# Optimization experiments

Measured on AMD Instinct MI355X. Metric: run time of the kernel, lower is better.

Reference implementation:

```python
import jax, jax.numpy as jnp
import numpy as np

B, SA, SB, H, D = 1, 2048, 512, 24, 128
DIM = H * D
EPS = 1e-6


def rms_norm(x, w):
    # fp32 variance as in the torch module (inputs already fp32 here)
    var = jnp.mean(jnp.square(x.astype(jnp.float32)), axis=-1, keepdims=True)
    y = (x * jax.lax.rsqrt(var + EPS)).astype(x.dtype)
    return y * w


def apply_rope(x, freqs):
    # x: [B,H,S,D]; freqs: [1,1,S,D/2,2,2]
    x_ = x.astype(jnp.float32).reshape(*x.shape[:-1], -1, 1, 2)  # [B,H,S,D/2,1,2]
    out = freqs[..., 0] * x_[..., 0] + freqs[..., 1] * x_[..., 1]  # [B,H,S,D/2,2]
    return out.reshape(x.shape).astype(x.dtype)


def qkv_split(x, W, b):
    # x: [B,S,DIM] -> q,k,v each [B,H,S,D]; chunk(3,dim=1) on 3H axis == major-3 split
    qkv = (x @ W + b).reshape(x.shape[0], x.shape[1], 3, H, D)
    qkv = jnp.transpose(qkv, (2, 0, 3, 1, 4))  # [3,B,H,S,D]
    return qkv[0], qkv[1], qkv[2]


def setup_inputs():
    key = jax.random.key(0)
    ks = jax.random.split(key, 8)
    s = 0.02
    return {
        "hidden_states_a": jax.random.normal(ks[0], (B, SA, DIM), jnp.float32),
        "hidden_states_b": jax.random.normal(ks[1], (B, SB, DIM), jnp.float32),
        "image_rotary_emb": jax.random.normal(ks[2], (1, 1, SA + SB, D // 2, 2, 2), jnp.float32),
        "Wqkv_a": jax.random.normal(ks[3], (DIM, 3 * DIM), jnp.float32) * s,
        "bqkv_a": jnp.zeros((3 * DIM,), jnp.float32),
        "Wqkv_b": jax.random.normal(ks[4], (DIM, 3 * DIM), jnp.float32) * s,
        "bqkv_b": jnp.zeros((3 * DIM,), jnp.float32),
        "wq_a": jnp.ones((D,), jnp.float32),
        "wk_a": jnp.ones((D,), jnp.float32),
        "wq_b": jnp.ones((D,), jnp.float32),
        "wk_b": jnp.ones((D,), jnp.float32),
        "Wout_a": jax.random.normal(ks[5], (DIM, DIM), jnp.float32) * s,
        "bout_a": jnp.zeros((DIM,), jnp.float32),
        "Wout_b": jax.random.normal(ks[6], (DIM, DIM), jnp.float32) * s,
        "bout_b": jnp.zeros((DIM,), jnp.float32),
    }


def reference(hidden_states_a, hidden_states_b, image_rotary_emb,
              Wqkv_a, bqkv_a, Wqkv_b, bqkv_b,
              wq_a, wk_a, wq_b, wk_b,
              Wout_a, bout_a, Wout_b, bout_b):
    q_a, k_a, v_a = qkv_split(hidden_states_a, Wqkv_a, bqkv_a)
    q_a, k_a = rms_norm(q_a, wq_a), rms_norm(k_a, wk_a)
    q_b, k_b, v_b = qkv_split(hidden_states_b, Wqkv_b, bqkv_b)
    q_b, k_b = rms_norm(q_b, wq_b), rms_norm(k_b, wk_b)

    q = jnp.concatenate([q_b, q_a], axis=2)
    k = jnp.concatenate([k_b, k_a], axis=2)
    v = jnp.concatenate([v_b, v_a], axis=2)
    q, k = apply_rope(q, image_rotary_emb), apply_rope(k, image_rotary_emb)

    scale = 1.0 / jnp.sqrt(jnp.asarray(D, q.dtype))
    scores = jnp.einsum("bhqd,bhkd->bhqk", q, k) * scale
    attn = jax.nn.softmax(scores, axis=-1)
    out = jnp.einsum("bhqk,bhkd->bhqd", attn, v)
    out = jnp.transpose(out, (0, 2, 1, 3)).reshape(B, SA + SB, DIM)

    out_b, out_a = out[:, :SB], out[:, SB:]
    hidden_states_a = out_a @ Wout_a + bout_a
    hidden_states_b = out_b @ Wout_b + bout_b
    return hidden_states_a, hidden_states_b
```

## Files before the change

### kernel.cpp

```cpp
#include <hip/hip_runtime.h>
#include <hip/hip_bf16.h>


typedef __attribute__((ext_vector_type(8))) short s16x8;
typedef __attribute__((ext_vector_type(8))) unsigned short u16x8;
typedef __attribute__((ext_vector_type(4))) float f32x4;
typedef __attribute__((ext_vector_type(16))) float f32x16;

#define DEV static __device__ __forceinline__

#define S_TOT 2560
#define DIMC 3072
#define NQKV 9216

DEV unsigned short f2bf(float f) {
  union { float f; unsigned u; } v; v.f = f;
  return (unsigned short)((v.u + 0x7fffu + ((v.u >> 16) & 1u)) >> 16);
}
DEV float bf2f(unsigned short h) {
  union { unsigned u; float f; } v; v.u = ((unsigned)h) << 16;
  return v.f;
}
DEV void gload16(const void* g, void* l) {
  __builtin_amdgcn_global_load_lds((__attribute__((address_space(1))) void*)g,
                                   (__attribute__((address_space(3))) void*)l,
                                   16, 0, 0);
}
DEV float exp2_fast(float x) {
#if __has_builtin(__builtin_amdgcn_exp2f)
  return __builtin_amdgcn_exp2f(x);
#else
  return __expf(x * 0.69314718056f);
#endif
}
template <int CTRL>
DEV float dppf(float x) {
  return __int_as_float(__builtin_amdgcn_update_dpp(0, __float_as_int(x), CTRL, 0xf, 0xf, true));
}
DEV float rowmax16(float x) {
  x = fmaxf(x, dppf<0xB1>(x));
  x = fmaxf(x, dppf<0x4E>(x));
  x = fmaxf(x, dppf<0x141>(x));
  x = fmaxf(x, dppf<0x140>(x));
  return x;
}
DEV float rowsum16(float x) {
  x += dppf<0xB1>(x);
  x += dppf<0x4E>(x);
  x += dppf<0x141>(x);
  x += dppf<0x140>(x);
  return x;
}

DEV void tile_map(int t, int mgrid, int* m, int* n) {
  int sg = t >> 4, loc = t & 15;
  int mgs = mgrid >> 2;
  int mg = sg % mgs, ng = sg / mgs;
  *m = mg * 4 + (loc & 3);
  *n = ng * 4 + (loc >> 2);
}


__global__ __launch_bounds__(256) void cvt_bf16_k(const float* __restrict__ in,
                                                  unsigned short* __restrict__ out,
                                                  int n8) {
  int i = blockIdx.x * 256 + threadIdx.x;
  if (i >= n8) return;
  const float4* p = (const float4*)(in + (size_t)i * 8);
  float4 a = p[0], b = p[1];
  u16x8 u;
  u[0] = f2bf(a.x); u[1] = f2bf(a.y); u[2] = f2bf(a.z); u[3] = f2bf(a.w);
  u[4] = f2bf(b.x); u[5] = f2bf(b.y); u[6] = f2bf(b.z); u[7] = f2bf(b.w);
  *(u16x8*)(out + (size_t)i * 8) = u;
}

__global__ __launch_bounds__(256) void transpose_cvt(const float* __restrict__ W,
                                                     unsigned short* __restrict__ WT,
                                                     int K, int N) {
  __shared__ float tile[64][65];
  const int t = threadIdx.x;
  const int n0 = blockIdx.x * 64, k0 = blockIdx.y * 64;
#pragma unroll
  for (int rep = 0; rep < 4; ++rep) {
    int idx = rep * 256 + t;
    int r = idx >> 4, c4 = (idx & 15) * 4;
    float4 v = *(const float4*)&W[(size_t)(k0 + r) * N + n0 + c4];
    tile[r][c4] = v.x; tile[r][c4 + 1] = v.y; tile[r][c4 + 2] = v.z; tile[r][c4 + 3] = v.w;
  }
  __syncthreads();
#pragma unroll
  for (int rep = 0; rep < 2; ++rep) {
    int idx = rep * 256 + t;
    int j = idx >> 3, i0 = (idx & 7) * 8;
    u16x8 u;
#pragma unroll
    for (int i = 0; i < 8; i++) u[i] = f2bf(tile[i0 + i][j]);
    *(u16x8*)&WT[(size_t)(n0 + j) * K + k0 + i0] = u;
  }
}


struct StageSmem {
  unsigned short A[128 * 64];
  unsigned short B[128 * 64];
};

DEV void stage_tile(const char* A, const char* B, StageSmem* s, int kt, int tid) {
  const int row_s = tid >> 3;
  const int kbp = (tid & 7) * 16;
#pragma unroll
  for (int st = 0; st < 4; ++st) {
    int row = st * 32 + row_s;
    int kb = kbp ^ ((row & 7) << 4);
    gload16(A + (size_t)row * (DIMC * 2) + kt * 128 + kb, (char*)s->A + st * 4096 + tid * 16);
    gload16(B + (size_t)row * (DIMC * 2) + kt * 128 + kb, (char*)s->B + st * 4096 + tid * 16);
  }
}

DEV void gemm_core(const unsigned short* __restrict__ Ap,
                   const unsigned short* __restrict__ Bp,
                   StageSmem (&sm)[2], int tid, f32x4 (&acc)[4][4]) {
  const int wave = tid >> 6, lane = tid & 63;
  const int wr = wave >> 1, wc = wave & 1;
  const int lh = lane >> 4, ll = lane & 15;

  stage_tile((const char*)Ap, (const char*)Bp, &sm[0], 0, tid);
  __syncthreads();

  for (int kt = 0; kt < 48; ++kt) {
    if (kt + 1 < 48)
      stage_tile((const char*)Ap, (const char*)Bp, &sm[(kt + 1) & 1], kt + 1, tid);
    const StageSmem* s = &sm[kt & 1];
#pragma unroll
    for (int ks = 0; ks < 2; ++ks) {
      s16x8 a[4], b[4];
#pragma unroll
      for (int f = 0; f < 4; ++f) {
        int ar = wr * 64 + f * 16 + ll;
        a[f] = *(const s16x8*)((const char*)s->A + ar * 128 +
                               ((ks * 64 + lh * 16) ^ ((ar & 7) << 4)));
        int br = wc * 64 + f * 16 + ll;
        b[f] = *(const s16x8*)((const char*)s->B + br * 128 +
                               ((ks * 64 + lh * 16) ^ ((br & 7) << 4)));
      }
#pragma unroll
      for (int i = 0; i < 4; i++)
#pragma unroll
        for (int j = 0; j < 4; j++)
          acc[i][j] = __builtin_amdgcn_mfma_f32_16x16x32_bf16(a[i], b[j], acc[i][j], 0, 0, 0);
    }
    __syncthreads();
  }
}


union QkvSmem {
  StageSmem st[2];
  unsigned short ctile[128 * 136];
};

__global__ __launch_bounds__(256, 2) void qkv_gemm(
    const unsigned short* __restrict__ X0, const unsigned short* __restrict__ X1,
    const unsigned short* __restrict__ W0, const unsigned short* __restrict__ W1,
    const float* __restrict__ b0, const float* __restrict__ b1,
    const float* __restrict__ wqa, const float* __restrict__ wka,
    const float* __restrict__ wqb, const float* __restrict__ wkb,
    const float* __restrict__ freqs,
    unsigned short* __restrict__ Qb, unsigned short* __restrict__ Kb,
    unsigned short* __restrict__ Vt, int nt0) {
  __shared__ QkvSmem sm;
  const int tid = threadIdx.x;

  const int chunk = gridDim.x >> 3;
  const int nid = ((int)blockIdx.x & 7) * chunk + ((int)blockIdx.x >> 3);
  const int strm = (nid >= nt0) ? 1 : 0;
  const int t = strm ? nid - nt0 : nid;
  int mt, nt;
  tile_map(t, strm ? 4 : 16, &mt, &nt);
  const int m0 = mt * 128, n0 = nt * 128;
  const unsigned short* Xp = (strm ? X1 : X0) + (size_t)m0 * DIMC;
  const unsigned short* Wp = (strm ? W1 : W0) + (size_t)n0 * DIMC;
  const float* biasp = (strm ? b1 : b0);
  const int s_off = strm ? 0 : 512;

  f32x4 acc[4][4] = {};
  gemm_core(Xp, Wp, sm.st, tid, acc);

  {
    const int wave = tid >> 6, lane = tid & 63;
    const int wr = wave >> 1, wc = wave & 1, lh = lane >> 4, ll = lane & 15;
#pragma unroll
    for (int fn = 0; fn < 4; ++fn) {
      int c = wc * 64 + fn * 16 + ll;
      float bv = biasp[n0 + c];
#pragma unroll
      for (int fm = 0; fm < 4; ++fm)
#pragma unroll
        for (int j = 0; j < 4; j++) {
          int r = wr * 64 + fm * 16 + lh * 4 + j;
          sm.ctile[r * 136 + c] = f2bf(acc[fm][fn][j] + bv);
        }
    }
  }
  __syncthreads();

  const int qkv_idx = nt / 24;
  const int head = nt % 24;

  if (qkv_idx == 2) {
    const int sg0 = s_off + m0;
#pragma unroll
    for (int half = 0; half < 2; ++half) {
      int d = half * 64 + (tid >> 2);
      int t0 = (tid & 3) * 32;
      size_t obase = (size_t)(head * 128 + d) * S_TOT + sg0 + t0;
#pragma unroll
      for (int v = 0; v < 4; ++v) {
        u16x8 u;
#pragma unroll
        for (int i = 0; i < 8; i++) u[i] = sm.ctile[(t0 + v * 8 + i) * 136 + d];
        *(u16x8*)&Vt[obase + v * 8] = u;
      }
    }
  } else {
    const float* wn = (qkv_idx == 0) ? (strm ? wqb : wqa) : (strm ? wkb : wka);
    unsigned short* Ob = (qkv_idx == 0) ? Qb : Kb;
    const int row = tid >> 1, half = tid & 1;
    const int sg = s_off + m0 + row;
    float x[64];
    float ss = 0.f;
#pragma unroll
    for (int i = 0; i < 64; i++) {
      float v = bf2f(sm.ctile[row * 136 + half * 64 + i]);
      x[i] = v; ss += v * v;
    }
    ss += __shfl_xor(ss, 1);
    const float rn = rsqrtf(ss * (1.f / 128.f) + 1e-6f);
    const float* fr = freqs + (size_t)sg * 256 + half * 128;
    unsigned short o[64];
#pragma unroll
    for (int p = 0; p < 32; ++p) {
      float w0 = wn[half * 64 + 2 * p], w1 = wn[half * 64 + 2 * p + 1];
      float y0 = x[2 * p] * rn * w0, y1 = x[2 * p + 1] * rn * w1;
      float f00 = fr[p * 4], f01 = fr[p * 4 + 1], f10 = fr[p * 4 + 2], f11 = fr[p * 4 + 3];
      o[2 * p] = f2bf(f00 * y0 + f01 * y1);
      o[2 * p + 1] = f2bf(f10 * y0 + f11 * y1);
    }
    size_t ob = ((size_t)head * S_TOT + sg) * 128 + half * 64;
#pragma unroll
    for (int v = 0; v < 8; ++v) {
      u16x8 u;
#pragma unroll
      for (int i = 0; i < 8; i++) u[i] = o[v * 8 + i];
      *(u16x8*)&Ob[ob + v * 8] = u;
    }
  }
}


__global__ __launch_bounds__(256, 2) void out_gemm(
    const unsigned short* __restrict__ A0, const unsigned short* __restrict__ A1,
    const unsigned short* __restrict__ W0, const unsigned short* __restrict__ W1,
    const float* __restrict__ b0, const float* __restrict__ b1,
    float* __restrict__ C0, float* __restrict__ C1, int nt0) {
  __shared__ StageSmem sm[2];
  const int tid = threadIdx.x;
  const int chunk = gridDim.x >> 3;
  const int nid = ((int)blockIdx.x & 7) * chunk + ((int)blockIdx.x >> 3);
  const int strm = (nid >= nt0) ? 1 : 0;
  const int t = strm ? nid - nt0 : nid;
  int mt, nt;
  tile_map(t, strm ? 4 : 16, &mt, &nt);
  const int m0 = mt * 128, n0 = nt * 128;
  const unsigned short* Ap = (strm ? A1 : A0) + (size_t)m0 * DIMC;
  const unsigned short* Wp = (strm ? W1 : W0) + (size_t)n0 * DIMC;
  const float* bias = strm ? b1 : b0;
  float* C = strm ? C1 : C0;

  f32x4 acc[4][4] = {};
  gemm_core(Ap, Wp, sm, tid, acc);
  const int wave = tid >> 6, lane = tid & 63;
  const int wr = wave >> 1, wc = wave & 1, lh = lane >> 4, ll = lane & 15;
#pragma unroll
  for (int fn = 0; fn < 4; ++fn) {
    int c = n0 + wc * 64 + fn * 16 + ll;
    float bv = bias[c];
#pragma unroll
    for (int fm = 0; fm < 4; ++fm)
#pragma unroll
      for (int j = 0; j < 4; j++) {
        int r = m0 + wr * 64 + fm * 16 + lh * 4 + j;
        C[(size_t)r * DIMC + c] = acc[fm][fn][j] + bv;
      }
  }
}


__global__ __launch_bounds__(256, 2) void attn_k(
    const unsigned short* __restrict__ Qb, const unsigned short* __restrict__ Kb,
    const unsigned short* __restrict__ Vt, unsigned short* __restrict__ AO) {
  __shared__ alignas(128) unsigned short Ks[2][64 * 128];
  __shared__ alignas(128) unsigned short Vs[128 * 64];
  __shared__ alignas(128) unsigned short Ps[4][32 * 72];
  __shared__ float tabA[4][32];
  __shared__ float tabL[4][32];

  const int tid = threadIdx.x, w = tid >> 6, lane = tid & 63;
  const int lh = lane >> 4, ll16 = lane & 15;
  const int ll31 = lane & 31, hi = lane >> 5;
  const int wgid = blockIdx.x;
  const int nid = (wgid & 7) * 60 + (wgid >> 3);
  const int h = nid / 20, qt = nid % 20;
  const float C = 0.12751744f;

  s16x8 qf[2][4];
#pragma unroll
  for (int rb = 0; rb < 2; rb++) {
    size_t qbase = ((size_t)h * S_TOT + qt * 128 + w * 32 + rb * 16 + ll16) * 128;
#pragma unroll
    for (int ks = 0; ks < 4; ks++) qf[rb][ks] = *(const s16x8*)&Qb[qbase + ks * 32 + lh * 8];
  }

  float m2[2][4], l_r[2][4];
  f32x16 o[4] = {};
#pragma unroll
  for (int rb = 0; rb < 2; rb++)
#pragma unroll
    for (int j = 0; j < 4; j++) { m2[rb][j] = -1e30f; l_r[rb][j] = 0.f; }

  const unsigned short* Kh = Kb + (size_t)h * S_TOT * 128;
  const unsigned short* Vh = Vt + (size_t)h * 128 * S_TOT;
  unsigned short* Pw = &Ps[w][0];

  {
#pragma unroll
    for (int st = 0; st < 4; ++st) {
      int row = st * 16 + (tid >> 4);
      int col = ((tid & 15) * 16) ^ ((row & 7) << 4);
      gload16((const char*)(Kh + (size_t)row * 128) + col,
              (char*)&Ks[0][0] + st * 4096 + tid * 16);
    }
  }

  int cur = 0;
  for (int kt = 0; kt < 40; ++kt) {
    __syncthreads();
    {
      const int k0 = kt * 64;
#pragma unroll
      for (int st = 0; st < 4; ++st) {
        int row = st * 32 + (tid >> 3);
        int col = ((tid & 7) * 16) ^ ((row & 7) << 4);
        gload16((const char*)(Vh + (size_t)row * S_TOT + k0) + col,
                (char*)Vs + st * 4096 + tid * 16);
      }
    }
    if (kt + 1 < 40) {
      const unsigned short* Kn = Kh + (size_t)(kt + 1) * 64 * 128;
#pragma unroll
      for (int st = 0; st < 4; ++st) {
        int row = st * 16 + (tid >> 4);
        int col = ((tid & 15) * 16) ^ ((row & 7) << 4);
        gload16((const char*)(Kn + (size_t)row * 128) + col,
                (char*)&Ks[cur ^ 1][0] + st * 4096 + tid * 16);
      }
    }

    const char* Kc = (const char*)&Ks[cur][0];
    f32x4 sc[2][4] = {};
#pragma unroll
    for (int kb = 0; kb < 4; kb++) {
      int krow = kb * 16 + ll16;
      const char* kr = Kc + krow * 256;
      int swz = (krow & 7) << 4;
#pragma unroll
      for (int ks = 0; ks < 4; ks++) {
        s16x8 bf = *(const s16x8*)(kr + ((ks * 64 + lh * 16) ^ swz));
        sc[0][kb] = __builtin_amdgcn_mfma_f32_16x16x32_bf16(qf[0][ks], bf, sc[0][kb], 0, 0, 0);
        sc[1][kb] = __builtin_amdgcn_mfma_f32_16x16x32_bf16(qf[1][ks], bf, sc[1][kb], 0, 0, 0);
      }
    }

    float pmax[2][4];
#pragma unroll
    for (int rb = 0; rb < 2; rb++)
#pragma unroll
      for (int j = 0; j < 4; j++) {
        float v = fmaxf(fmaxf(sc[rb][0][j], sc[rb][1][j]), fmaxf(sc[rb][2][j], sc[rb][3][j]));
        pmax[rb][j] = rowmax16(v) * C;
      }
    bool need = false;
#pragma unroll
    for (int rb = 0; rb < 2; rb++)
#pragma unroll
      for (int j = 0; j < 4; j++) need |= (pmax[rb][j] > m2[rb][j] + 8.0f);
    if (__any(need)) {
#pragma unroll
      for (int rb = 0; rb < 2; rb++)
#pragma unroll
        for (int j = 0; j < 4; j++) {
          float mn = fmaxf(m2[rb][j], pmax[rb][j]);
          float al = exp2_fast(m2[rb][j] - mn);
          m2[rb][j] = mn;
          l_r[rb][j] *= al;
          if (ll16 == 0) tabA[w][rb * 16 + lh * 4 + j] = al;
        }
#pragma unroll
      for (int reg = 0; reg < 16; reg++) {
        int cr = (reg & 3) + 8 * (reg >> 2) + 4 * hi;
        float alv = tabA[w][cr];
        o[0][reg] *= alv; o[1][reg] *= alv; o[2][reg] *= alv; o[3][reg] *= alv;
      }
    }
#pragma unroll
    for (int rb = 0; rb < 2; rb++) {
      float ps0 = 0.f, ps1 = 0.f, ps2 = 0.f, ps3 = 0.f;
#pragma unroll
      for (int kb = 0; kb < 4; kb++) {
        float p0 = exp2_fast(sc[rb][kb][0] * C - m2[rb][0]);
        float p1 = exp2_fast(sc[rb][kb][1] * C - m2[rb][1]);
        float p2 = exp2_fast(sc[rb][kb][2] * C - m2[rb][2]);
        float p3 = exp2_fast(sc[rb][kb][3] * C - m2[rb][3]);
        ps0 += p0; ps1 += p1; ps2 += p2; ps3 += p3;
        int rbase = (rb * 16 + lh * 4);
        Pw[(rbase + 0) * 72 + kb * 16 + ll16] = f2bf(p0);
        Pw[(rbase + 1) * 72 + kb * 16 + ll16] = f2bf(p1);
        Pw[(rbase + 2) * 72 + kb * 16 + ll16] = f2bf(p2);
        Pw[(rbase + 3) * 72 + kb * 16 + ll16] = f2bf(p3);
      }
      l_r[rb][0] += rowsum16(ps0);
      l_r[rb][1] += rowsum16(ps1);
      l_r[rb][2] += rowsum16(ps2);
      l_r[rb][3] += rowsum16(ps3);
    }

    __syncthreads();

#pragma unroll
    for (int kstep = 0; kstep < 4; kstep++) {
      s16x8 pa = *(const s16x8*)((const char*)Pw + ll31 * 144 + kstep * 32 + hi * 16);
#pragma unroll
      for (int dblk = 0; dblk < 4; dblk++) {
        int vrow = dblk * 32 + ll31;
        s16x8 vb = *(const s16x8*)((const char*)Vs + vrow * 128 +
                                   ((kstep * 32 + hi * 16) ^ ((vrow & 7) << 4)));
        o[dblk] = __builtin_amdgcn_mfma_f32_32x32x16_bf16(pa, vb, o[dblk], 0, 0, 0);
      }
    }
    cur ^= 1;
  }

  if (ll16 == 0) {
#pragma unroll
    for (int rb = 0; rb < 2; rb++)
#pragma unroll
      for (int j = 0; j < 4; j++) tabL[w][rb * 16 + lh * 4 + j] = l_r[rb][j];
  }
#pragma unroll
  for (int reg = 0; reg < 16; reg++) {
    int cr = (reg & 3) + 8 * (reg >> 2) + 4 * hi;
    float inv = 1.0f / tabL[w][cr];
    int srow = qt * 128 + w * 32 + cr;
    size_t base = (size_t)srow * DIMC + h * 128;
#pragma unroll
    for (int dblk = 0; dblk < 4; dblk++)
      AO[base + dblk * 32 + ll31] = f2bf(o[dblk][reg] * inv);
  }
}


extern "C" void kernel_launch(void* const* d_in, const int* in_sizes, int n_in,
                              void* d_out, int out_size, void* d_ws, size_t ws_size,
                              hipStream_t stream) {
  (void)in_sizes; (void)n_in; (void)out_size; (void)ws_size;
  const float* Xa = (const float*)d_in[0];
  const float* Xb = (const float*)d_in[1];
  const float* freqs = (const float*)d_in[2];
  const float* Wqkv_a = (const float*)d_in[3];
  const float* bqkv_a = (const float*)d_in[4];
  const float* Wqkv_b = (const float*)d_in[5];
  const float* bqkv_b = (const float*)d_in[6];
  const float* wq_a = (const float*)d_in[7];
  const float* wk_a = (const float*)d_in[8];
  const float* wq_b = (const float*)d_in[9];
  const float* wk_b = (const float*)d_in[10];
  const float* Wout_a = (const float*)d_in[11];
  const float* bout_a = (const float*)d_in[12];
  const float* Wout_b = (const float*)d_in[13];
  const float* bout_b = (const float*)d_in[14];
  float* out = (float*)d_out;

  char* ws = (char*)d_ws;
  unsigned short* WTa  = (unsigned short*)ws; ws += (size_t)NQKV * DIMC * 2;
  unsigned short* WTb  = (unsigned short*)ws; ws += (size_t)NQKV * DIMC * 2;
  unsigned short* WoTa = (unsigned short*)ws; ws += (size_t)DIMC * DIMC * 2;
  unsigned short* WoTb = (unsigned short*)ws; ws += (size_t)DIMC * DIMC * 2;
  unsigned short* Xa16 = (unsigned short*)ws; ws += (size_t)2048 * DIMC * 2;
  unsigned short* Xb16 = (unsigned short*)ws; ws += (size_t)512 * DIMC * 2;
  unsigned short* Qb   = (unsigned short*)ws; ws += (size_t)24 * S_TOT * 128 * 2;
  unsigned short* Kbf  = (unsigned short*)ws; ws += (size_t)24 * S_TOT * 128 * 2;
  unsigned short* Vt   = (unsigned short*)ws; ws += (size_t)24 * S_TOT * 128 * 2;
  unsigned short* AO   = (unsigned short*)ws; ws += (size_t)S_TOT * DIMC * 2;

  cvt_bf16_k<<<dim3(2048 * DIMC / 8 / 256), dim3(256), 0, stream>>>(Xa, Xa16, 2048 * DIMC / 8);
  cvt_bf16_k<<<dim3(512 * DIMC / 8 / 256), dim3(256), 0, stream>>>(Xb, Xb16, 512 * DIMC / 8);
  transpose_cvt<<<dim3(NQKV / 64, DIMC / 64), dim3(256), 0, stream>>>(Wqkv_a, WTa, DIMC, NQKV);
  transpose_cvt<<<dim3(NQKV / 64, DIMC / 64), dim3(256), 0, stream>>>(Wqkv_b, WTb, DIMC, NQKV);
  transpose_cvt<<<dim3(DIMC / 64, DIMC / 64), dim3(256), 0, stream>>>(Wout_a, WoTa, DIMC, DIMC);
  transpose_cvt<<<dim3(DIMC / 64, DIMC / 64), dim3(256), 0, stream>>>(Wout_b, WoTb, DIMC, DIMC);

  qkv_gemm<<<dim3(1440), dim3(256), 0, stream>>>(Xa16, Xb16, WTa, WTb, bqkv_a, bqkv_b,
                                                 wq_a, wk_a, wq_b, wk_b, freqs,
                                                 Qb, Kbf, Vt, 1152);

  attn_k<<<dim3(480), dim3(256), 0, stream>>>(Qb, Kbf, Vt, AO);

  out_gemm<<<dim3(480), dim3(256), 0, stream>>>(AO + (size_t)512 * DIMC, AO, WoTa, WoTb,
                                                bout_a, bout_b, out,
                                                out + (size_t)2048 * DIMC, 384);
}
```

Measured before the change: 482.1 us.

## Merge prep kernels, single-buffer QKV GEMM, relax attention barriers

Fuses the two input-conversion launches into one kernel and the four weight transpose launches into one, removing per-launch overhead. The QKV GEMM switches from double-buffered to single-buffered LDS staging, sized to 48KB, which shrinks shared memory and may improve occupancy but exposes load latency. The attention kernel replaces __syncthreads with explicit vmcnt waits plus a raw barrier, so the prefetch of the next K/V tile can stay in flight across the first barrier. The vmcnt counts are hand-picked and depend on how many loads are outstanding, which risks races if those counts are wrong.

```diff
diff --git a/kernel.cpp b/kernel.cpp
--- a/kernel.cpp
+++ b/kernel.cpp
@@ -26,6 +26,8 @@
                                    (__attribute__((address_space(3))) void*)l,
                                    16, 0, 0);
 }
+template <int N>
+DEV void wait_vm() { asm volatile("s_waitcnt vmcnt(%0)" :: "n"(N) : "memory"); }
 DEV float exp2_fast(float x) {
 #if __has_builtin(__builtin_amdgcn_exp2f)
   return __builtin_amdgcn_exp2f(x);
@@ -61,11 +63,15 @@
 }
 
 
-__global__ __launch_bounds__(256) void cvt_bf16_k(const float* __restrict__ in,
-                                                  unsigned short* __restrict__ out,
-                                                  int n8) {
+__global__ __launch_bounds__(256) void cvt_both(const float* __restrict__ Xa,
+                                                const float* __restrict__ Xb,
+                                                unsigned short* __restrict__ Oa,
+                                                unsigned short* __restrict__ Ob,
+                                                int n8a, int n8b) {
   int i = blockIdx.x * 256 + threadIdx.x;
-  if (i >= n8) return;
+  const float* in; unsigned short* out;
+  if (i < n8a) { in = Xa; out = Oa; }
+  else { i -= n8a; if (i >= n8b) return; in = Xb; out = Ob; }
   const float4* p = (const float4*)(in + (size_t)i * 8);
   float4 a = p[0], b = p[1];
   u16x8 u;
@@ -74,12 +80,20 @@
   *(u16x8*)(out + (size_t)i * 8) = u;
 }
 
-__global__ __launch_bounds__(256) void transpose_cvt(const float* __restrict__ W,
-                                                     unsigned short* __restrict__ WT,
-                                                     int K, int N) {
+__global__ __launch_bounds__(256) void transpose_all(
+    const float* __restrict__ Wqa, const float* __restrict__ Wqb,
+    const float* __restrict__ Woa, const float* __restrict__ Wob,
+    unsigned short* __restrict__ Tqa, unsigned short* __restrict__ Tqb,
+    unsigned short* __restrict__ Toa, unsigned short* __restrict__ Tob) {
   __shared__ float tile[64][65];
+  int id = blockIdx.x;
+  const float* W; unsigned short* WT; int N, ncols;
+  if (id < 6912)        { W = Wqa; WT = Tqa; N = NQKV; ncols = 144; }
+  else if (id < 13824)  { W = Wqb; WT = Tqb; N = NQKV; ncols = 144; id -= 6912; }
+  else if (id < 16128)  { W = Woa; WT = Toa; N = DIMC; ncols = 48;  id -= 13824; }
+  else                  { W = Wob; WT = Tob; N = DIMC; ncols = 48;  id -= 16128; }
   const int t = threadIdx.x;
-  const int n0 = blockIdx.x * 64, k0 = blockIdx.y * 64;
+  const int n0 = (id % ncols) * 64, k0 = (id / ncols) * 64;
 #pragma unroll
   for (int rep = 0; rep < 4; ++rep) {
     int idx = rep * 256 + t;
@@ -95,7 +109,7 @@
     u16x8 u;
 #pragma unroll
     for (int i = 0; i < 8; i++) u[i] = f2bf(tile[i0 + i][j]);
-    *(u16x8*)&WT[(size_t)(n0 + j) * K + k0 + i0] = u;
+    *(u16x8*)&WT[(size_t)(n0 + j) * DIMC + k0 + i0] = u;
   }
 }
 
@@ -117,46 +131,64 @@
   }
 }
 
-DEV void gemm_core(const unsigned short* __restrict__ Ap,
-                   const unsigned short* __restrict__ Bp,
-                   StageSmem (&sm)[2], int tid, f32x4 (&acc)[4][4]) {
+DEV void compute_tile(const StageSmem* s, int wr, int wc, int lh, int ll,
+                      f32x4 (&acc)[4][4]) {
+#pragma unroll
+  for (int ks = 0; ks < 2; ++ks) {
+    s16x8 a[4], b[4];
+#pragma unroll
+    for (int f = 0; f < 4; ++f) {
+      int ar = wr * 64 + f * 16 + ll;
+      a[f] = *(const s16x8*)((const char*)s->A + ar * 128 +
+                             ((ks * 64 + lh * 16) ^ ((ar & 7) << 4)));
+      int br = wc * 64 + f * 16 + ll;
+      b[f] = *(const s16x8*)((const char*)s->B + br * 128 +
+                             ((ks * 64 + lh * 16) ^ ((br & 7) << 4)));
+    }
+#pragma unroll
+    for (int i = 0; i < 4; i++)
+#pragma unroll
+      for (int j = 0; j < 4; j++)
+        acc[i][j] = __builtin_amdgcn_mfma_f32_16x16x32_bf16(a[i], b[j], acc[i][j], 0, 0, 0);
+  }
+}
+
+DEV void gemm_core_sb(const unsigned short* __restrict__ Ap,
+                      const unsigned short* __restrict__ Bp,
+                      StageSmem* s, int tid, f32x4 (&acc)[4][4]) {
   const int wave = tid >> 6, lane = tid & 63;
   const int wr = wave >> 1, wc = wave & 1;
   const int lh = lane >> 4, ll = lane & 15;
+  for (int kt = 0; kt < 48; ++kt) {
+    stage_tile((const char*)Ap, (const char*)Bp, s, kt, tid);
+    __syncthreads();
+    compute_tile(s, wr, wc, lh, ll, acc);
+    __syncthreads();
+  }
+}
+
+DEV void gemm_core_db(const unsigned short* __restrict__ Ap,
+                      const unsigned short* __restrict__ Bp,
+                      StageSmem (&sm)[2], int tid, f32x4 (&acc)[4][4]) {
+  const int wave = tid >> 6, lane = tid & 63;
+  const int wr = wave >> 1, wc = wave & 1;
+  const int lh = lane >> 4, ll = lane & 15;
 
   stage_tile((const char*)Ap, (const char*)Bp, &sm[0], 0, tid);
   __syncthreads();
-
   for (int kt = 0; kt < 48; ++kt) {
     if (kt + 1 < 48)
       stage_tile((const char*)Ap, (const char*)Bp, &sm[(kt + 1) & 1], kt + 1, tid);
-    const StageSmem* s = &sm[kt & 1];
-#pragma unroll
-    for (int ks = 0; ks < 2; ++ks) {
-      s16x8 a[4], b[4];
-#pragma unroll
-      for (int f = 0; f < 4; ++f) {
-        int ar = wr * 64 + f * 16 + ll;
-        a[f] = *(const s16x8*)((const char*)s->A + ar * 128 +
-                               ((ks * 64 + lh * 16) ^ ((ar & 7) << 4)));
-        int br = wc * 64 + f * 16 + ll;
-        b[f] = *(const s16x8*)((const char*)s->B + br * 128 +
-                               ((ks * 64 + lh * 16) ^ ((br & 7) << 4)));
-      }
-#pragma unroll
-      for (int i = 0; i < 4; i++)
-#pragma unroll
-        for (int j = 0; j < 4; j++)
-          acc[i][j] = __builtin_amdgcn_mfma_f32_16x16x32_bf16(a[i], b[j], acc[i][j], 0, 0, 0);
-    }
+    compute_tile(&sm[kt & 1], wr, wc, lh, ll, acc);
     __syncthreads();
   }
 }
 
 
 union QkvSmem {
-  StageSmem st[2];
+  StageSmem st;
   unsigned short ctile[128 * 136];
+  char pad[49152];
 };
 
 __global__ __launch_bounds__(256, 2) void qkv_gemm(
@@ -184,7 +216,7 @@
   const int s_off = strm ? 0 : 512;
 
   f32x4 acc[4][4] = {};
-  gemm_core(Xp, Wp, sm.st, tid, acc);
+  gemm_core_sb(Xp, Wp, &sm.st, tid, acc);
 
   {
     const int wave = tid >> 6, lane = tid & 63;
@@ -278,7 +310,7 @@
   float* C = strm ? C1 : C0;
 
   f32x4 acc[4][4] = {};
-  gemm_core(Ap, Wp, sm, tid, acc);
+  gemm_core_db(Ap, Wp, sm, tid, acc);
   const int wave = tid >> 6, lane = tid & 63;
   const int wr = wave >> 1, wc = wave & 1, lh = lane >> 4, ll = lane & 15;
 #pragma unroll
@@ -344,7 +376,8 @@
 
   int cur = 0;
   for (int kt = 0; kt < 40; ++kt) {
-    __syncthreads();
+    wait_vm<0>();
+    __builtin_amdgcn_s_barrier();
     {
       const int k0 = kt * 64;
 #pragma unroll
@@ -434,7 +467,8 @@
       l_r[rb][3] += rowsum16(ps3);
     }
 
-    __syncthreads();
+    if (kt + 1 < 40) wait_vm<16>(); else wait_vm<0>();
+    __builtin_amdgcn_s_barrier();
 
 #pragma unroll
     for (int kstep = 0; kstep < 4; kstep++) {
@@ -502,12 +536,10 @@
   unsigned short* Vt   = (unsigned short*)ws; ws += (size_t)24 * S_TOT * 128 * 2;
   unsigned short* AO   = (unsigned short*)ws; ws += (size_t)S_TOT * DIMC * 2;
 
-  cvt_bf16_k<<<dim3(2048 * DIMC / 8 / 256), dim3(256), 0, stream>>>(Xa, Xa16, 2048 * DIMC / 8);
-  cvt_bf16_k<<<dim3(512 * DIMC / 8 / 256), dim3(256), 0, stream>>>(Xb, Xb16, 512 * DIMC / 8);
-  transpose_cvt<<<dim3(NQKV / 64, DIMC / 64), dim3(256), 0, stream>>>(Wqkv_a, WTa, DIMC, NQKV);
-  transpose_cvt<<<dim3(NQKV / 64, DIMC / 64), dim3(256), 0, stream>>>(Wqkv_b, WTb, DIMC, NQKV);
-  transpose_cvt<<<dim3(DIMC / 64, DIMC / 64), dim3(256), 0, stream>>>(Wout_a, WoTa, DIMC, DIMC);
-  transpose_cvt<<<dim3(DIMC / 64, DIMC / 64), dim3(256), 0, stream>>>(Wout_b, WoTb, DIMC, DIMC);
+  const int n8a = 2048 * DIMC / 8, n8b = 512 * DIMC / 8;
+  cvt_both<<<dim3((n8a + n8b) / 256), dim3(256), 0, stream>>>(Xa, Xb, Xa16, Xb16, n8a, n8b);
+  transpose_all<<<dim3(18432), dim3(256), 0, stream>>>(Wqkv_a, Wqkv_b, Wout_a, Wout_b,
+                                                       WTa, WTb, WoTa, WoTb);
 
   qkv_gemm<<<dim3(1440), dim3(256), 0, stream>>>(Xa16, Xb16, WTa, WTb, bqkv_a, bqkv_b,
                                                  wq_a, wk_a, wq_b, wk_b, freqs,
```

After: 495.5 us. +2.8%, slower.
